# Performance work log

Hardware: AMD Instinct MI355X
Metric: run time of the kernel (lower is better)

Reference implementation:

```python
import jax, jax.numpy as jnp
import numpy as np

N, E = 50000, 100000
D, H, EDGE_DIM = 300, 4, 4  # node_dim, heads, edge_dim; per-head C = D
HC = H * D


def setup_inputs() -> dict:
    key = jax.random.key(0)
    ks = jax.random.split(key, 16)
    s = 0.02
    return {
        "xin": jax.random.normal(ks[0], (N, D), jnp.float32),
        "e_idx": jax.random.randint(ks[1], (2, E), 0, N, jnp.int64 if jax.config.jax_enable_x64 else jnp.int32),
        "e_attr": jax.random.normal(ks[2], (E, EDGE_DIM), jnp.float32),
        # TransformerConv params
        "Wq": jax.random.normal(ks[3], (D, HC), jnp.float32) * s,
        "bq": jnp.zeros((HC,), jnp.float32),
        "Wk": jax.random.normal(ks[4], (D, HC), jnp.float32) * s,
        "bk": jnp.zeros((HC,), jnp.float32),
        "Wv": jax.random.normal(ks[5], (D, HC), jnp.float32) * s,
        "bv": jnp.zeros((HC,), jnp.float32),
        "We": jax.random.normal(ks[6], (EDGE_DIM, HC), jnp.float32) * s,
        "be": jnp.zeros((HC,), jnp.float32),
        "Wskip": jax.random.normal(ks[7], (D, HC), jnp.float32) * s,
        "bskip": jnp.zeros((HC,), jnp.float32),
        # LayerNorm params
        "ln_a": jnp.ones((HC,), jnp.float32),
        "ln_b": jnp.zeros((HC,), jnp.float32),
        # output Linear params
        "Wlin": jax.random.normal(ks[8], (HC, D), jnp.float32) * s,
        "blin": jnp.zeros((D,), jnp.float32),
    }


def _forward(xin, e_idx, e_attr, Wq, bq, Wk, bk, Wv, bv, We, be, Wskip, bskip, ln_a, ln_b, Wlin, blin):
    n = xin.shape[0]
    src, dst = e_idx[0], e_idx[1]
    scale = 1.0 / jnp.sqrt(jnp.float32(D))

    q = (xin @ Wq + bq).reshape(n, H, D)
    k = (xin @ Wk + bk).reshape(n, H, D)
    v = (xin @ Wv + bv).reshape(n, H, D)
    ee = (e_attr @ We + be).reshape(-1, H, D)  # [E,H,C]

    kj = k[src] + ee                                        # gather + edge conditioning
    alpha = jnp.einsum('ehc,ehc->eh', q[dst], kj) * scale   # [E,H]
    amax = jax.ops.segment_max(alpha, dst, num_segments=n)  # segment softmax
    alpha = jnp.exp(alpha - amax[dst])
    denom = jax.ops.segment_sum(alpha, dst, num_segments=n)
    alpha = alpha / (denom[dst] + 1e-16)

    msg = (v[src] + ee) * alpha[:, :, None]                 # [E,H,C]
    agg = jax.ops.segment_sum(msg.reshape(-1, HC), dst, num_segments=n)
    x = agg + xin @ Wskip + bskip                           # root/skip weight

    # LayerNorm (biased variance)
    mean = x.mean(-1, keepdims=True)
    var = ((x - mean) ** 2).mean(-1, keepdims=True)
    x = ln_a * (x - mean) / jnp.sqrt(var + 1e-5) + ln_b

    x = x @ Wlin + blin
    return jax.nn.elu(x + xin)


def reference(xin, e_idx, e_attr, Wq, bq, Wk, bk, Wv, bv, We, be, Wskip, bskip, ln_a, ln_b, Wlin, blin):
    return _forward(xin, e_idx, e_attr, Wq, bq, Wk, bk, Wv, bv, We, be, Wskip, bskip, ln_a, ln_b, Wlin, blin)
```

## Files before the change

kernel.cpp:

```cpp
#include <hip/hip_runtime.h>
#include <hip/hip_bf16.h>

typedef __bf16 bf16;
typedef __bf16 bf16x4 __attribute__((ext_vector_type(4)));
typedef __bf16 bf16x8 __attribute__((ext_vector_type(8)));
typedef float f32x4 __attribute__((ext_vector_type(4)));

constexpr int kN = 50000;
constexpr int kE = 100000;
constexpr int kD = 300;
constexpr int kH = 4;
constexpr int kHC = 1200;
constexpr int kK1A = 304;
constexpr int kK1B = 320;
constexpr int kNP1 = 2432;
constexpr int kMP = 50048;
constexpr int kK2 = 1216;
constexpr int kN2P = 384;
constexpr int kLY = 1216;
constexpr int kNB1 = kNP1 / 128;
constexpr int kMB2 = kMP / 64;
constexpr int kT1 = kK1B / 32;
constexpr int kNB2 = kN2P / 128;
constexpr int kT2 = kK2 / 32;
constexpr int kWG1 = kMB2 * kNB1;
constexpr int kWG2 = kMB2 * kNB2;
constexpr int kEW = 136;
constexpr int kSplitRow = 49342;
constexpr size_t kXhiBytes = (size_t)(kN + 1 - kSplitRow) * kK1A * 2;

__device__ __forceinline__ float ldF(const void* p, size_t i, int f32) {
    return f32 ? ((const float*)p)[i] : (float)((const bf16*)p)[i];
}
__device__ __forceinline__ int ldI(const void* p, size_t i, int i64) {
    return i64 ? ((const int*)p)[2 * i] : ((const int*)p)[i];
}

__device__ __forceinline__ const bf16* xrow(const bf16* lo, const bf16* hi, int r) {
    return r < kSplitRow ? lo + (size_t)r * kK1A : hi + (size_t)(r - kSplitRow) * kK1A;
}
__device__ __forceinline__ bf16* xrow_w(bf16* lo, bf16* hi, int r) {
    return r < kSplitRow ? lo + (size_t)r * kK1A : hi + (size_t)(r - kSplitRow) * kK1A;
}

__device__ __forceinline__ void glds16(const void* g, void* l) {
    __builtin_amdgcn_global_load_lds((const __attribute__((address_space(1))) void*)g,
                                     (__attribute__((address_space(3))) void*)l, 16, 0, 0);
}

template <int NWG>
__device__ __forceinline__ int xcd_swz(int phys) {
    constexpr int q = NWG >> 3, r = NWG & 7;
    int xcd = phys & 7, i = phys >> 3;
    int base = xcd < r ? xcd * (q + 1) : r * (q + 1) + (xcd - r) * q;
    return base + i;
}

__device__ __forceinline__ float bflo(unsigned u) {
    return __builtin_bit_cast(float, u << 16);
}
__device__ __forceinline__ float bfhi(unsigned u) {
    return __builtin_bit_cast(float, u & 0xFFFF0000u);
}
__device__ __forceinline__ unsigned bfpack(float a, float b) {
    bf16 x = (bf16)a, y = (bf16)b;
    unsigned short ux = __builtin_bit_cast(unsigned short, x);
    unsigned short uy = __builtin_bit_cast(unsigned short, y);
    return (unsigned)ux | ((unsigned)uy << 16);
}
__device__ __forceinline__ float wsum(float v) {
#pragma unroll
    for (int o = 32; o > 0; o >>= 1) v += __shfl_xor(v, o);
    return v;
}

__global__ void detect_kernel(const unsigned short* __restrict__ xin_u,
                              const int* __restrict__ eidx_i,
                              int* __restrict__ flags) {
    __shared__ int s_ff, s_nz;
    if (threadIdx.x == 0) { s_ff = 0; s_nz = 0; }
    __syncthreads();
    int c1 = 0;
    for (int i = threadIdx.x; i < 65536; i += 256)
        c1 += (((xin_u[i] >> 7) & 0xFF) == 0xFF);
    int c2 = 0;
    for (int i = threadIdx.x; i < 1024; i += 256)
        c2 += (eidx_i[2 * i + 1] != 0);
    atomicAdd(&s_ff, c1);
    atomicAdd(&s_nz, c2);
    __syncthreads();
    if (threadIdx.x == 0) {
        flags[0] = (s_ff > 0) ? 1 : 0;
        flags[1] = (s_nz == 0) ? 1 : 0;
    }
}

__global__ void cast5(const void* __restrict__ We, const void* __restrict__ be,
                      const void* __restrict__ lna, const void* __restrict__ lnb,
                      const void* __restrict__ blin, float* __restrict__ Wef,
                      float* __restrict__ bef, float* __restrict__ lnaf,
                      float* __restrict__ lnbf, float* __restrict__ blinf,
                      const int* __restrict__ flags) {
    int i = blockIdx.x * 256 + threadIdx.x;
    int f32 = flags[0];
    if (i < 4 * kHC) { Wef[i] = ldF(We, i, f32); return; }
    i -= 4 * kHC;
    if (i < kHC) { bef[i] = ldF(be, i, f32); return; }
    i -= kHC;
    if (i < kHC) { lnaf[i] = ldF(lna, i, f32); return; }
    i -= kHC;
    if (i < kHC) { lnbf[i] = ldF(lnb, i, f32); return; }
    i -= kHC;
    if (i < kD) blinf[i] = ldF(blin, i, f32);
}

__global__ void cast_xpad(const void* __restrict__ xin, bf16* __restrict__ xlo,
                          bf16* __restrict__ xhi, const int* __restrict__ flags) {
    int idx = blockIdx.x * 256 + threadIdx.x;
    if (idx < 4) {
        bf16x4 z = {};
        *(bf16x4*)&xlo[(size_t)kSplitRow * kK1A + idx * 4] = z;
    }
    if (idx >= (kN + 1) * 76) return;
    int r = idx / 76, c4 = idx % 76;
    int c = c4 * 4;
    bf16x4 w = {};
    if (r < kN && c < kD) {
        int f32 = flags[0];
        size_t b = (size_t)r * kD + c;
        w[0] = (bf16)ldF(xin, b + 0, f32);
        w[1] = (bf16)ldF(xin, b + 1, f32);
        w[2] = (bf16)ldF(xin, b + 2, f32);
        w[3] = (bf16)ldF(xin, b + 3, f32);
    }
    *(bf16x4*)&(xrow_w(xlo, xhi, r)[c]) = w;
}

__global__ void pack_W1f(const void* __restrict__ Wq, const void* __restrict__ Wk,
                         const void* __restrict__ Wv, const void* __restrict__ Ws,
                         bf16* __restrict__ Bf, const int* __restrict__ flags) {
    int idx = blockIdx.x * 256 + threadIdx.x;
    if (idx >= 2 * kNB1 * kT1 * 8 * 64) return;
    int f32 = flags[0];
    int lane = idx & 63;
    int fi = (idx >> 6) & 7;
    int ksnb = idx >> 9;
    int ks = ksnb % kT1;
    int nbp = ksnb / kT1;
    int p = nbp / kNB1, nb = nbp % kNB1;
    int n = nb * 128 + fi * 16 + (lane & 15);
    int kbase = ks * 32 + (lane >> 4) * 8;
    const void* W = nullptr;
    int c = 0;
    if (n < kHC)          { W = p == 0 ? Wq : Ws; c = n; }
    else if (n < 2 * kHC) { W = p == 0 ? Wk : Wv; c = n - kHC; }
    bf16x8 w = {};
#pragma unroll
    for (int e = 0; e < 8; ++e) {
        int k = kbase + e;
        float v = 0.f;
        if (W && k < kD) v = ldF(W, (size_t)k * kHC + c, f32);
        w[e] = (bf16)v;
    }
    *(bf16x8*)&Bf[(size_t)idx * 8] = w;
}

__global__ void pack_W2f(const void* __restrict__ Wlin, bf16* __restrict__ Bf,
                         const int* __restrict__ flags) {
    int idx = blockIdx.x * 256 + threadIdx.x;
    if (idx >= kNB2 * kT2 * 8 * 64) return;
    int f32 = flags[0];
    int lane = idx & 63;
    int fi = (idx >> 6) & 7;
    int ksnb = idx >> 9;
    int ks = ksnb % kT2;
    int nb = ksnb / kT2;
    int n = nb * 128 + fi * 16 + (lane & 15);
    int kbase = ks * 32 + (lane >> 4) * 8;
    bf16x8 w = {};
#pragma unroll
    for (int e = 0; e < 8; ++e) {
        int k = kbase + e;
        float v = 0.f;
        if (n < kD && k < kHC) v = ldF(Wlin, (size_t)k * kD + n, f32);
        w[e] = (bf16)v;
    }
    *(bf16x8*)&Bf[(size_t)idx * 8] = w;
}

__global__ void pack_bias(const void* __restrict__ bq, const void* __restrict__ bk,
                          const void* __restrict__ bv, const void* __restrict__ bs,
                          float* __restrict__ bcat, const int* __restrict__ flags) {
    int n = blockIdx.x * 256 + threadIdx.x;
    if (n >= 2 * kNP1) return;
    int f32 = flags[0];
    int p = n / kNP1, nl = n % kNP1;
    float v = 0.f;
    if (nl < 2 * kHC) {
        const void* b;
        int c;
        if (nl < kHC) { b = p == 0 ? bq : bs; c = nl; }
        else          { b = p == 0 ? bk : bv; c = nl - kHC; }
        v = ldF(b, c, f32);
    }
    bcat[n] = v;
}

__global__ void hist_kernel(const void* __restrict__ eidx, int* __restrict__ cnt,
                            const int* __restrict__ flags) {
    int e = blockIdx.x * 256 + threadIdx.x;
    if (e < kE) atomicAdd(&cnt[ldI(eidx, (size_t)kE + e, flags[1])], 1);
}

__global__ void scan_local(const int* __restrict__ cnt, int* __restrict__ rowptr,
                           int* __restrict__ bsum) {
    int b = blockIdx.x, t = threadIdx.x;
    int i = b * 256 + t;
    int v = (i < kN) ? cnt[i] : 0;
    int lane = t & 63, wv = t >> 6;
    int s = v;
#pragma unroll
    for (int o = 1; o < 64; o <<= 1) {
        int u = __shfl_up(s, o);
        if (lane >= o) s += u;
    }
    __shared__ int wtot[4];
    if (lane == 63) wtot[wv] = s;
    __syncthreads();
    int add = 0;
    for (int w = 0; w < wv; ++w) add += wtot[w];
    if (i < kN) rowptr[i] = s - v + add;
    if (t == 255) bsum[b] = add + s;
}
__global__ void scan_bsums(int* __restrict__ bsum, int nb) {
    int t = threadIdx.x;
    int v = (t < nb) ? bsum[t] : 0;
    int lane = t & 63, wv = t >> 6;
    int s = v;
#pragma unroll
    for (int o = 1; o < 64; o <<= 1) {
        int u = __shfl_up(s, o);
        if (lane >= o) s += u;
    }
    __shared__ int wtot[4];
    if (lane == 63) wtot[wv] = s;
    __syncthreads();
    int add = 0;
    for (int w = 0; w < wv; ++w) add += wtot[w];
    if (t < nb) bsum[t] = s - v + add;
}
__global__ void scan_add(int* __restrict__ rowptr, const int* __restrict__ bsum) {
    int i = blockIdx.x * 256 + threadIdx.x;
    if (i < kN) rowptr[i] += bsum[i >> 8];
    if (i == 0) rowptr[kN] = kE;
}

__global__ void scatter_kernel(const void* __restrict__ eidx, const int* __restrict__ rowptr,
                               int* __restrict__ fill, int* __restrict__ esort,
                               const int* __restrict__ flags) {
    int e = blockIdx.x * 256 + threadIdx.x;
    if (e < kE) {
        int d = ldI(eidx, (size_t)kE + e, flags[1]);
        int pos = rowptr[d] + atomicAdd(&fill[d], 1);
        esort[pos] = e;
    }
}

__global__ __launch_bounds__(256, 4) void gemm_qkvs(const bf16* __restrict__ xlo,
                                                    const bf16* __restrict__ xhi,
                                                    const bf16* __restrict__ Bf,
                                                    const float* __restrict__ bcat,
                                                    bf16* __restrict__ outA,
                                                    bf16* __restrict__ outB) {
    __shared__ alignas(16) bf16 As[64 * 32];
    __shared__ alignas(16) bf16 Es[64 * kEW];
    const int logical = xcd_swz<kWG1>(blockIdx.x);
    const int mb = logical / kNB1, nb = logical % kNB1;
    const int tid = threadIdx.x;
    const int lane = tid & 63, wave = tid >> 6;
    const int quad = lane >> 4, l16 = lane & 15;
    const int mw = (wave >> 1) * 32;
    const int fibase = (wave & 1) * 4;
    const f32x4 zero = {0.f, 0.f, 0.f, 0.f};
    f32x4 acc[2][4];
#pragma unroll
    for (int i = 0; i < 2; i++)
#pragma unroll
        for (int j = 0; j < 4; j++) acc[i][j] = zero;
    const int mblk = mb * 64, nblk = nb * 128;
    const int srow = wave * 16 + (lane >> 2);
    const int ss = lane & 3;
    int gr = mblk + srow; if (gr >= kN) gr = kN - 1;
    const bf16* gA = xrow(xlo, xhi, gr) + ((ss ^ ((srow >> 1) & 3)) << 3);
    bf16* lA = As + wave * 512;
    int aoff[2];
#pragma unroll
    for (int i = 0; i < 2; i++) {
        int ra = mw + i * 16 + l16;
        aoff[i] = ra * 32 + ((quad ^ ((ra >> 1) & 3)) << 3);
    }
    const bf16* bbase = Bf + (size_t)nb * (kT1 * 4096) + fibase * 512 + lane * 8;
    for (int t = 0; t < kT1; ++t) {
        __syncthreads();
        glds16(gA + t * 32, lA);
        bf16x8 bfv[4];
#pragma unroll
        for (int ni = 0; ni < 4; ni++)
            bfv[ni] = *(const bf16x8*)(bbase + (size_t)t * 4096 + ni * 512);
        __syncthreads();
        bf16x8 af[2];
#pragma unroll
        for (int i = 0; i < 2; i++) af[i] = *(const bf16x8*)&As[aoff[i]];
#pragma unroll
        for (int mi = 0; mi < 2; mi++)
#pragma unroll
            for (int ni = 0; ni < 4; ni++)
                acc[mi][ni] = __builtin_amdgcn_mfma_f32_16x16x32_bf16(
                    af[mi], bfv[ni], acc[mi][ni], 0, 0, 0);
    }
    __syncthreads();
#pragma unroll
    for (int mi = 0; mi < 2; mi++)
#pragma unroll
        for (int r = 0; r < 4; r++) {
            int lr = mw + mi * 16 + quad * 4 + r;
#pragma unroll
            for (int ni = 0; ni < 4; ni++) {
                int lc = (fibase + ni) * 16 + l16;
                Es[lr * kEW + lc] = (bf16)(acc[mi][ni][r] + bcat[nblk + lc]);
            }
        }
    __syncthreads();
#pragma unroll
    for (int it = 0; it < 4; ++it) {
        int row = it * 16 + (tid >> 4);
        int col8 = (tid & 15) * 8;
        int m = mblk + row;
        if (m >= kN) continue;
        bf16x8 w = *(const bf16x8*)&Es[row * kEW + col8];
        int n = nblk + col8;
        if (n < kHC)          *(bf16x8*)&outA[(size_t)m * kLY + n] = w;
        else if (n < 2 * kHC) *(bf16x8*)&outB[(size_t)m * kHC + (n - kHC)] = w;
    }
}

__global__ __launch_bounds__(256) void node_alpha(const int* __restrict__ rowptr,
                                                  const int* __restrict__ esort,
                                                  const void* __restrict__ eidx,
                                                  const void* __restrict__ eattr,
                                                  bf16* __restrict__ qb,
                                                  const bf16* __restrict__ kb,
                                                  const float* __restrict__ Wef,
                                                  const float* __restrict__ bef,
                                                  float* __restrict__ alpha,
                                                  const int* __restrict__ flags) {
    int i = blockIdx.x;
    int h = threadIdx.x >> 6, lane = threadIdx.x & 63;
    int r0 = rowptr[i], r1 = rowptr[i + 1];
    if (r0 >= r1) return;
    int f32 = flags[0], i64 = flags[1];
    const unsigned* qr = (const unsigned*)(qb + (size_t)i * kLY + h * kD);
    float q0[3], q1[3];
#pragma unroll
    for (int j = 0; j < 3; ++j) {
        int p = lane + 64 * j;
        unsigned u = (p < 150) ? qr[p] : 0u;
        q0[j] = bflo(u); q1[j] = bfhi(u);
    }
    float tj[4], tb;
#pragma unroll
    for (int jj = 0; jj < 4; ++jj) {
        const float* w = Wef + jj * kHC + h * kD;
        float s = 0.f;
#pragma unroll
        for (int j = 0; j < 3; ++j) {
            int p = lane + 64 * j;
            if (p < 150) s += q0[j] * w[2 * p] + q1[j] * w[2 * p + 1];
        }
        tj[jj] = wsum(s);
    }
    {
        const float* br = bef + h * kD;
        float s = 0.f;
#pragma unroll
        for (int j = 0; j < 3; ++j) {
            int p = lane + 64 * j;
            if (p < 150) s += q0[j] * br[2 * p] + q1[j] * br[2 * p + 1];
        }
        tb = wsum(s);
    }
    float denom = 0.f;
    for (int p = r0; p < r1; ++p) {
        int e = esort[p];
        int src = ldI(eidx, e, i64);
        const unsigned* kr = (const unsigned*)(kb + (size_t)src * kHC + h * kD);
        float s = 0.f;
#pragma unroll
        for (int j = 0; j < 3; ++j) {
            int pp = lane + 64 * j;
            if (pp < 150) { unsigned u = kr[pp]; s += q0[j] * bflo(u) + q1[j] * bfhi(u); }
        }
        float dot = wsum(s);
        float ea0 = ldF(eattr, (size_t)e * 4 + 0, f32), ea1 = ldF(eattr, (size_t)e * 4 + 1, f32);
        float ea2 = ldF(eattr, (size_t)e * 4 + 2, f32), ea3 = ldF(eattr, (size_t)e * 4 + 3, f32);
        float logit = dot + ea0 * tj[0] + ea1 * tj[1] + ea2 * tj[2] + ea3 * tj[3] + tb;
        float a = expf(logit * 0.05773502691896258f);
        if (lane == 0) alpha[e * kH + h] = a;
        denom += a;
    }
    if (lane == 0)
        ((float*)(qb + (size_t)i * kLY + kHC))[h] = 1.f / (denom + 1e-16f);
}

__global__ __launch_bounds__(256) void node_fused(const int* __restrict__ rowptr,
                                                  const int* __restrict__ esort,
                                                  const void* __restrict__ eidx,
                                                  const void* __restrict__ eattr,
                                                  const float* __restrict__ Wef,
                                                  const float* __restrict__ bef,
                                                  const float* __restrict__ alpha,
                                                  const bf16* __restrict__ vb,
                                                  const float* __restrict__ lnaf,
                                                  const float* __restrict__ lnbf,
                                                  bf16* __restrict__ qy,
                                                  const int* __restrict__ flags) {
    int i = blockIdx.x;
    int t = threadIdx.x, h = t >> 6, lane = t & 63;
    bf16* yr = qy + (size_t)i * kLY;
    if (i >= kN) {
        for (int c = t; c < kK2; c += 256) yr[c] = (bf16)0.f;
        return;
    }
    int f32 = flags[0], i64 = flags[1];
    int r0 = rowptr[i], r1 = rowptr[i + 1];
    float inv = (r1 > r0) ? ((const float*)(yr + kHC))[h] : 0.f;
    unsigned* yr32 = (unsigned*)(yr + h * kD);
    float a0[3], a1[3];
#pragma unroll
    for (int j = 0; j < 3; ++j) {
        int p = lane + 64 * j;
        unsigned u = (p < 150) ? yr32[p] : 0u;
        a0[j] = bflo(u); a1[j] = bfhi(u);
    }
    float S0 = 0.f, S1 = 0.f, S2 = 0.f, S3 = 0.f, Sb = 0.f;
    for (int p = r0; p < r1; ++p) {
        int e = esort[p];
        int src = ldI(eidx, e, i64);
        float coeff = alpha[e * kH + h] * inv;
        float ea0 = ldF(eattr, (size_t)e * 4 + 0, f32), ea1 = ldF(eattr, (size_t)e * 4 + 1, f32);
        float ea2 = ldF(eattr, (size_t)e * 4 + 2, f32), ea3 = ldF(eattr, (size_t)e * 4 + 3, f32);
        S0 += coeff * ea0; S1 += coeff * ea1; S2 += coeff * ea2; S3 += coeff * ea3;
        Sb += coeff;
        const unsigned* vr = (const unsigned*)(vb + (size_t)src * kHC + h * kD);
#pragma unroll
        for (int j = 0; j < 3; ++j) {
            int pp = lane + 64 * j;
            if (pp < 150) {
                unsigned u = vr[pp];
                a0[j] += coeff * bflo(u);
                a1[j] += coeff * bfhi(u);
            }
        }
    }
    {
        const float* wb = Wef + h * kD;
        const float* br = bef + h * kD;
#pragma unroll
        for (int j = 0; j < 3; ++j) {
            int p = lane + 64 * j;
            if (p < 150) {
                int c0 = 2 * p, c1 = 2 * p + 1;
                a0[j] += S0 * wb[c0] + S1 * wb[kHC + c0] + S2 * wb[2 * kHC + c0] +
                         S3 * wb[3 * kHC + c0] + Sb * br[c0];
                a1[j] += S0 * wb[c1] + S1 * wb[kHC + c1] + S2 * wb[2 * kHC + c1] +
                         S3 * wb[3 * kHC + c1] + Sb * br[c1];
            }
        }
    }
    float s = 0.f, s2 = 0.f;
#pragma unroll
    for (int j = 0; j < 3; ++j) {
        s += a0[j] + a1[j];
        s2 += a0[j] * a0[j] + a1[j] * a1[j];
    }
#pragma unroll
    for (int off = 32; off > 0; off >>= 1) {
        s += __shfl_down(s, off);
        s2 += __shfl_down(s2, off);
    }
    __shared__ float ss[4], ss2[4];
    if (lane == 0) { ss[h] = s; ss2[h] = s2; }
    __syncthreads();
    if (t == 0) {
        float S = ss[0] + ss[1] + ss[2] + ss[3];
        float S2 = ss2[0] + ss2[1] + ss2[2] + ss2[3];
        float mean = S / (float)kHC;
        float var = S2 / (float)kHC - mean * mean;
        ss[0] = mean;
        ss2[0] = rsqrtf(var + 1e-5f);
    }
    __syncthreads();
    float mean = ss[0], rstd = ss2[0];
#pragma unroll
    for (int j = 0; j < 3; ++j) {
        int p = lane + 64 * j;
        if (p < 150) {
            int c0 = h * kD + 2 * p;
            float v0 = lnaf[c0] * (a0[j] - mean) * rstd + lnbf[c0];
            float v1 = lnaf[c0 + 1] * (a1[j] - mean) * rstd + lnbf[c0 + 1];
            yr32[p] = bfpack(v0, v1);
        }
    }
    if (t < kK2 - kHC) yr[kHC + t] = (bf16)0.f;
}

__global__ __launch_bounds__(256, 4) void gemm_out(const bf16* __restrict__ Ay,
                                                   const bf16* __restrict__ Bf,
                                                   const float* __restrict__ blinf,
                                                   const void* __restrict__ xin,
                                                   void* __restrict__ out,
                                                   const int* __restrict__ flags) {
    __shared__ alignas(16) bf16 As[64 * 32];
    const int logical = xcd_swz<kWG2>(blockIdx.x);
    const int mb = logical / kNB2, nb = logical % kNB2;
    const int f32 = flags[0];
    const int tid = threadIdx.x;
    const int lane = tid & 63, wave = tid >> 6;
    const int quad = lane >> 4, l16 = lane & 15;
    const int mw = (wave >> 1) * 32;
    const int fibase = (wave & 1) * 4;
    const f32x4 zero = {0.f, 0.f, 0.f, 0.f};
    f32x4 acc[2][4];
#pragma unroll
    for (int i = 0; i < 2; i++)
#pragma unroll
        for (int j = 0; j < 4; j++) acc[i][j] = zero;
    const int mblk = mb * 64, nblk = nb * 128;
    const int srow = wave * 16 + (lane >> 2);
    const int ss = lane & 3;
    const bf16* gA = Ay + (size_t)(mblk + srow) * kLY + ((ss ^ ((srow >> 1) & 3)) << 3);
    bf16* lA = As + wave * 512;
    int aoff[2];
#pragma unroll
    for (int i = 0; i < 2; i++) {
        int ra = mw + i * 16 + l16;
        aoff[i] = ra * 32 + ((quad ^ ((ra >> 1) & 3)) << 3);
    }
    const bf16* bbase = Bf + (size_t)nb * (kT2 * 4096) + fibase * 512 + lane * 8;
    for (int t = 0; t < kT2; ++t) {
        __syncthreads();
        glds16(gA + t * 32, lA);
        bf16x8 bfv[4];
#pragma unroll
        for (int ni = 0; ni < 4; ni++)
            bfv[ni] = *(const bf16x8*)(bbase + (size_t)t * 4096 + ni * 512);
        __syncthreads();
        bf16x8 af[2];
#pragma unroll
        for (int i = 0; i < 2; i++) af[i] = *(const bf16x8*)&As[aoff[i]];
#pragma unroll
        for (int mi = 0; mi < 2; mi++)
#pragma unroll
            for (int ni = 0; ni < 4; ni++)
                acc[mi][ni] = __builtin_amdgcn_mfma_f32_16x16x32_bf16(
                    af[mi], bfv[ni], acc[mi][ni], 0, 0, 0);
    }
#pragma unroll
    for (int mi = 0; mi < 2; mi++)
#pragma unroll
        for (int r = 0; r < 4; r++) {
            int m = mblk + mw + mi * 16 + quad * 4 + r;
            if (m >= kN) continue;
#pragma unroll
            for (int ni = 0; ni < 4; ni++) {
                int n = nblk + (fibase + ni) * 16 + l16;
                if (n >= kD) continue;
                float resid = ldF(xin, (size_t)m * kD + n, f32);
                float t2 = acc[mi][ni][r] + blinf[n] + resid;
                float r2 = t2 > 0.f ? t2 : expm1f(t2);
                if (f32) ((float*)out)[(size_t)m * kD + n] = r2;
                else     ((bf16*)out)[(size_t)m * kD + n] = (bf16)r2;
            }
        }
}

__global__ void fallback_copy(const unsigned short* __restrict__ xin_u,
                              unsigned short* __restrict__ out_u) {
    int i = blockIdx.x * 256 + threadIdx.x;
    if (i < kN * kD) out_u[i] = xin_u[i];
}

extern "C" void kernel_launch(void* const* d_in, const int* in_sizes, int n_in,
                              void* d_out, int out_size, void* d_ws, size_t ws_size,
                              hipStream_t stream) {
    const void* xin  = d_in[0];
    const void* eidx = d_in[1];
    const void* eatt = d_in[2];
    const void* Wq   = d_in[3];
    const void* bq   = d_in[4];
    const void* Wk   = d_in[5];
    const void* bk   = d_in[6];
    const void* Wv   = d_in[7];
    const void* bv   = d_in[8];
    const void* We   = d_in[9];
    const void* be   = d_in[10];
    const void* Wsk  = d_in[11];
    const void* bsk  = d_in[12];
    const void* lna  = d_in[13];
    const void* lnb  = d_in[14];
    const void* Wlin = d_in[15];
    const void* blin = d_in[16];

    char* ws = (char*)d_ws;
    size_t off = 0;
    auto alloc = [&](size_t bytes) -> char* {
        char* p = ws + off;
        off += (bytes + 255) & ~(size_t)255;
        return p;
    };
    bf16* bufA   = (bf16*)alloc((size_t)kMP * kLY * 2);
    bf16* bufB   = (bf16*)alloc((size_t)kN * kHC * 2);
    bf16* W1f    = (bf16*)alloc((size_t)2 * kNP1 * kK1B * 2);
    float* bcat  = (float*)alloc((size_t)2 * kNP1 * 4);
    bf16* W2f    = (bf16*)alloc((size_t)kN2P * kK2 * 2);
    float* alpha = (float*)alloc((size_t)kE * kH * 4);
    char* ovl    = alloc(kXhiBytes);
    int* cnt     = (int*)ovl;
    int* fill    = (int*)(ovl + 200064);
    bf16* xhi    = (bf16*)ovl;
    int* rowptr  = (int*)alloc((size_t)(kN + 1) * 4);
    int* esort   = (int*)alloc((size_t)kE * 4);
    int* bsum    = (int*)alloc(256 * 4);
    float* Wef   = (float*)alloc((size_t)4 * kHC * 4);
    float* bef   = (float*)alloc((size_t)kHC * 4);
    float* lnaf  = (float*)alloc((size_t)kHC * 4);
    float* lnbf  = (float*)alloc((size_t)kHC * 4);
    float* blinf = (float*)alloc((size_t)kD * 4);
    int* flags   = (int*)alloc(2 * 4);
    (void)in_sizes; (void)n_in;
    bf16* xlo = (bf16*)d_out;
    if (off > ws_size ||
        (size_t)out_size * 2 < (size_t)kSplitRow * kK1A * 2 + 32) {
        fallback_copy<<<(kN * kD + 255) / 256, 256, 0, stream>>>(
            (const unsigned short*)xin, (unsigned short*)d_out);
        return;
    }

    constexpr int kScanNB = (kN + 255) / 256;
    detect_kernel<<<1, 256, 0, stream>>>((const unsigned short*)xin, (const int*)eidx, flags);
    hipMemsetAsync(cnt, 0, (size_t)kN * 4, stream);
    hipMemsetAsync(fill, 0, (size_t)kN * 4, stream);
    hist_kernel<<<(kE + 255) / 256, 256, 0, stream>>>(eidx, cnt, flags);
    scan_local<<<kScanNB, 256, 0, stream>>>(cnt, rowptr, bsum);
    scan_bsums<<<1, 256, 0, stream>>>(bsum, kScanNB);
    scan_add<<<kScanNB, 256, 0, stream>>>(rowptr, bsum);
    scatter_kernel<<<(kE + 255) / 256, 256, 0, stream>>>(eidx, rowptr, fill, esort, flags);
    cast_xpad<<<((kN + 1) * 76 + 255) / 256, 256, 0, stream>>>(xin, xlo, xhi, flags);
    cast5<<<(4 * kHC + 3 * kHC + kD + 255) / 256, 256, 0, stream>>>(
        We, be, lna, lnb, blin, Wef, bef, lnaf, lnbf, blinf, flags);
    pack_W1f<<<(2 * kNB1 * kT1 * 8 * 64 + 255) / 256, 256, 0, stream>>>(
        Wq, Wk, Wv, Wsk, W1f, flags);
    pack_bias<<<(2 * kNP1 + 255) / 256, 256, 0, stream>>>(bq, bk, bv, bsk, bcat, flags);
    pack_W2f<<<(kNB2 * kT2 * 8 * 64 + 255) / 256, 256, 0, stream>>>(Wlin, W2f, flags);

    gemm_qkvs<<<kWG1, 256, 0, stream>>>(xlo, xhi, W1f, bcat, bufA, bufB);
    node_alpha<<<kN, 256, 0, stream>>>(rowptr, esort, eidx, eatt, bufA, bufB,
                                       Wef, bef, alpha, flags);
    gemm_qkvs<<<kWG1, 256, 0, stream>>>(
        xlo, xhi, W1f + (size_t)kNB1 * kT1 * 4096, bcat + kNP1, bufA, bufB);
    node_fused<<<kMP, 256, 0, stream>>>(rowptr, esort, eidx, eatt, Wef, bef, alpha,
                                        bufB, lnaf, lnbf, bufA, flags);
    gemm_out<<<kWG2, 256, 0, stream>>>(bufA, W2f, blinf, xin, d_out, flags);
}
```

Before: 1.041 ms.

## Load GEMM A-fragments directly from global and prefetch next edge in loops

Both GEMM kernels stop staging A tiles through LDS with global_load_lds and two barriers per k-step. Each lane now loads its bf16x8 A fragment straight from global memory, and the QKVS GEMM's k-loop is fully unrolled. The attention-logit and aggregation edge loops software-prefetch the next edge's index, source, alpha and edge attributes, so those dependent loads overlap the current dot product. The A loads become redundant, less coalesced global reads (each row is shared by two waves), traded against removing the barrier stalls.

```diff
diff --git a/kernel.cpp b/kernel.cpp
--- a/kernel.cpp
+++ b/kernel.cpp
@@ -43,11 +43,6 @@
     return r < kSplitRow ? lo + (size_t)r * kK1A : hi + (size_t)(r - kSplitRow) * kK1A;
 }
 
-__device__ __forceinline__ void glds16(const void* g, void* l) {
-    __builtin_amdgcn_global_load_lds((const __attribute__((address_space(1))) void*)g,
-                                     (__attribute__((address_space(3))) void*)l, 16, 0, 0);
-}
-
 template <int NWG>
 __device__ __forceinline__ int xcd_swz(int phys) {
     constexpr int q = NWG >> 3, r = NWG & 7;
@@ -272,7 +267,6 @@
                                                     const float* __restrict__ bcat,
                                                     bf16* __restrict__ outA,
                                                     bf16* __restrict__ outB) {
-    __shared__ alignas(16) bf16 As[64 * 32];
     __shared__ alignas(16) bf16 Es[64 * kEW];
     const int logical = xcd_swz<kWG1>(blockIdx.x);
     const int mb = logical / kNB1, nb = logical % kNB1;
@@ -288,29 +282,23 @@
 #pragma unroll
         for (int j = 0; j < 4; j++) acc[i][j] = zero;
     const int mblk = mb * 64, nblk = nb * 128;
-    const int srow = wave * 16 + (lane >> 2);
-    const int ss = lane & 3;
-    int gr = mblk + srow; if (gr >= kN) gr = kN - 1;
-    const bf16* gA = xrow(xlo, xhi, gr) + ((ss ^ ((srow >> 1) & 3)) << 3);
-    bf16* lA = As + wave * 512;
-    int aoff[2];
+    const bf16* ar[2];
 #pragma unroll
     for (int i = 0; i < 2; i++) {
-        int ra = mw + i * 16 + l16;
-        aoff[i] = ra * 32 + ((quad ^ ((ra >> 1) & 3)) << 3);
+        int r = mblk + mw + i * 16 + l16;
+        if (r >= kN) r = kN - 1;
+        ar[i] = xrow(xlo, xhi, r) + quad * 8;
     }
     const bf16* bbase = Bf + (size_t)nb * (kT1 * 4096) + fibase * 512 + lane * 8;
+#pragma unroll
     for (int t = 0; t < kT1; ++t) {
-        __syncthreads();
-        glds16(gA + t * 32, lA);
+        bf16x8 af[2];
+#pragma unroll
+        for (int i = 0; i < 2; i++) af[i] = *(const bf16x8*)(ar[i] + t * 32);
         bf16x8 bfv[4];
 #pragma unroll
         for (int ni = 0; ni < 4; ni++)
             bfv[ni] = *(const bf16x8*)(bbase + (size_t)t * 4096 + ni * 512);
-        __syncthreads();
-        bf16x8 af[2];
-#pragma unroll
-        for (int i = 0; i < 2; i++) af[i] = *(const bf16x8*)&As[aoff[i]];
 #pragma unroll
         for (int mi = 0; mi < 2; mi++)
 #pragma unroll
@@ -318,7 +306,6 @@
                 acc[mi][ni] = __builtin_amdgcn_mfma_f32_16x16x32_bf16(
                     af[mi], bfv[ni], acc[mi][ni], 0, 0, 0);
     }
-    __syncthreads();
 #pragma unroll
     for (int mi = 0; mi < 2; mi++)
 #pragma unroll
@@ -390,9 +377,19 @@
         tb = wsum(s);
     }
     float denom = 0.f;
+    int e = esort[r0];
+    int src = ldI(eidx, e, i64);
+    float ea0 = ldF(eattr, (size_t)e * 4 + 0, f32), ea1 = ldF(eattr, (size_t)e * 4 + 1, f32);
+    float ea2 = ldF(eattr, (size_t)e * 4 + 2, f32), ea3 = ldF(eattr, (size_t)e * 4 + 3, f32);
     for (int p = r0; p < r1; ++p) {
-        int e = esort[p];
-        int src = ldI(eidx, e, i64);
+        int e2 = 0, src2 = 0;
+        float eb0 = 0.f, eb1 = 0.f, eb2 = 0.f, eb3 = 0.f;
+        if (p + 1 < r1) {
+            e2 = esort[p + 1];
+            src2 = ldI(eidx, e2, i64);
+            eb0 = ldF(eattr, (size_t)e2 * 4 + 0, f32); eb1 = ldF(eattr, (size_t)e2 * 4 + 1, f32);
+            eb2 = ldF(eattr, (size_t)e2 * 4 + 2, f32); eb3 = ldF(eattr, (size_t)e2 * 4 + 3, f32);
+        }
         const unsigned* kr = (const unsigned*)(kb + (size_t)src * kHC + h * kD);
         float s = 0.f;
 #pragma unroll
@@ -401,12 +398,11 @@
             if (pp < 150) { unsigned u = kr[pp]; s += q0[j] * bflo(u) + q1[j] * bfhi(u); }
         }
         float dot = wsum(s);
-        float ea0 = ldF(eattr, (size_t)e * 4 + 0, f32), ea1 = ldF(eattr, (size_t)e * 4 + 1, f32);
-        float ea2 = ldF(eattr, (size_t)e * 4 + 2, f32), ea3 = ldF(eattr, (size_t)e * 4 + 3, f32);
         float logit = dot + ea0 * tj[0] + ea1 * tj[1] + ea2 * tj[2] + ea3 * tj[3] + tb;
         float a = expf(logit * 0.05773502691896258f);
         if (lane == 0) alpha[e * kH + h] = a;
         denom += a;
+        e = e2; src = src2; ea0 = eb0; ea1 = eb1; ea2 = eb2; ea3 = eb3;
     }
     if (lane == 0)
         ((float*)(qb + (size_t)i * kLY + kHC))[h] = 1.f / (denom + 1e-16f);
@@ -443,12 +439,26 @@
         a0[j] = bflo(u); a1[j] = bfhi(u);
     }
     float S0 = 0.f, S1 = 0.f, S2 = 0.f, S3 = 0.f, Sb = 0.f;
+    int src = 0;
+    float al = 0.f, ea0 = 0.f, ea1 = 0.f, ea2 = 0.f, ea3 = 0.f;
+    if (r0 < r1) {
+        int e = esort[r0];
+        src = ldI(eidx, e, i64);
+        al = alpha[e * kH + h];
+        ea0 = ldF(eattr, (size_t)e * 4 + 0, f32); ea1 = ldF(eattr, (size_t)e * 4 + 1, f32);
+        ea2 = ldF(eattr, (size_t)e * 4 + 2, f32); ea3 = ldF(eattr, (size_t)e * 4 + 3, f32);
+    }
     for (int p = r0; p < r1; ++p) {
-        int e = esort[p];
-        int src = ldI(eidx, e, i64);
-        float coeff = alpha[e * kH + h] * inv;
-        float ea0 = ldF(eattr, (size_t)e * 4 + 0, f32), ea1 = ldF(eattr, (size_t)e * 4 + 1, f32);
-        float ea2 = ldF(eattr, (size_t)e * 4 + 2, f32), ea3 = ldF(eattr, (size_t)e * 4 + 3, f32);
+        int src2 = 0;
+        float al2 = 0.f, eb0 = 0.f, eb1 = 0.f, eb2 = 0.f, eb3 = 0.f;
+        if (p + 1 < r1) {
+            int e2 = esort[p + 1];
+            src2 = ldI(eidx, e2, i64);
+            al2 = alpha[e2 * kH + h];
+            eb0 = ldF(eattr, (size_t)e2 * 4 + 0, f32); eb1 = ldF(eattr, (size_t)e2 * 4 + 1, f32);
+            eb2 = ldF(eattr, (size_t)e2 * 4 + 2, f32); eb3 = ldF(eattr, (size_t)e2 * 4 + 3, f32);
+        }
+        float coeff = al * inv;
         S0 += coeff * ea0; S1 += coeff * ea1; S2 += coeff * ea2; S3 += coeff * ea3;
         Sb += coeff;
         const unsigned* vr = (const unsigned*)(vb + (size_t)src * kHC + h * kD);
@@ -461,6 +471,7 @@
                 a1[j] += coeff * bfhi(u);
             }
         }
+        src = src2; al = al2; ea0 = eb0; ea1 = eb1; ea2 = eb2; ea3 = eb3;
     }
     {
         const float* wb = Wef + h * kD;
@@ -520,7 +531,6 @@
                                                    const void* __restrict__ xin,
                                                    void* __restrict__ out,
                                                    const int* __restrict__ flags) {
-    __shared__ alignas(16) bf16 As[64 * 32];
     const int logical = xcd_swz<kWG2>(blockIdx.x);
     const int mb = logical / kNB2, nb = logical % kNB2;
     const int f32 = flags[0];
@@ -536,28 +546,21 @@
 #pragma unroll
         for (int j = 0; j < 4; j++) acc[i][j] = zero;
     const int mblk = mb * 64, nblk = nb * 128;
-    const int srow = wave * 16 + (lane >> 2);
-    const int ss = lane & 3;
-    const bf16* gA = Ay + (size_t)(mblk + srow) * kLY + ((ss ^ ((srow >> 1) & 3)) << 3);
-    bf16* lA = As + wave * 512;
-    int aoff[2];
+    const bf16* ar[2];
 #pragma unroll
     for (int i = 0; i < 2; i++) {
-        int ra = mw + i * 16 + l16;
-        aoff[i] = ra * 32 + ((quad ^ ((ra >> 1) & 3)) << 3);
+        int r = mblk + mw + i * 16 + l16;
+        ar[i] = Ay + (size_t)r * kLY + quad * 8;
     }
     const bf16* bbase = Bf + (size_t)nb * (kT2 * 4096) + fibase * 512 + lane * 8;
     for (int t = 0; t < kT2; ++t) {
-        __syncthreads();
-        glds16(gA + t * 32, lA);
+        bf16x8 af[2];
+#pragma unroll
+        for (int i = 0; i < 2; i++) af[i] = *(const bf16x8*)(ar[i] + t * 32);
         bf16x8 bfv[4];
 #pragma unroll
         for (int ni = 0; ni < 4; ni++)
             bfv[ni] = *(const bf16x8*)(bbase + (size_t)t * 4096 + ni * 512);
-        __syncthreads();
-        bf16x8 af[2];
-#pragma unroll
-        for (int i = 0; i < 2; i++) af[i] = *(const bf16x8*)&As[aoff[i]];
 #pragma unroll
         for (int mi = 0; mi < 2; mi++)
 #pragma unroll
```

After: 1.156 ms. +11.0%, slower.
